# Performance work log

Measured on AMD Instinct MI355X. Metric: run time of the kernel, lower is better.

The kernel has to match this reference:

```python
import jax, jax.numpy as jnp
import numpy as np

B, S, E, H = 2, 2048, 1024, 16
D = E // H  # head dim = 64

def setup_inputs() -> dict:
    key = jax.random.key(0)
    ks = jax.random.split(key, 7)
    mk = lambda k, shape, scale=1.0: (jax.random.normal(k, shape, dtype=jnp.float32) * scale)
    return {
        "query": mk(ks[0], (B, S, E)),
        "key": mk(ks[1], (B, S, E)),
        "value": mk(ks[2], (B, S, E)),
        "Wq": mk(ks[3], (E, E), 1.0 / np.sqrt(E)),
        "Wk": mk(ks[4], (E, E), 1.0 / np.sqrt(E)),
        "Wv": mk(ks[5], (E, E), 1.0 / np.sqrt(E)),
        "Wo": mk(ks[6], (E, E), 1.0 / np.sqrt(E)),
    }

def reference(query, key, value, Wq, Wk, Wv, Wo):
    # nn.Linear(bias=False): y = x @ W.T
    def split_heads(x):
        return x.reshape(B, -1, H, D).transpose(0, 2, 1, 3)  # [B,H,S,D]
    q = split_heads(query @ Wq.T)
    k = split_heads(key @ Wk.T)
    v = split_heads(value @ Wv.T)
    scores = jnp.einsum("bhqd,bhkd->bhqk", q, k) / jnp.sqrt(jnp.float32(D))
    attn = jax.nn.softmax(scores, axis=-1)  # dropout p=0 -> identity
    out = jnp.einsum("bhqk,bhkd->bhqd", attn, v)
    out = out.transpose(0, 2, 1, 3).reshape(B, -1, E)
    out = out @ Wo.T
    return out
```

## Files before the change

kernel.cpp:

```cpp
#include <hip/hip_runtime.h>
#include <stdint.h>

#define S_LEN 2048
#define HDIM  64
#define EMB   1024
#define NTOK  4096

typedef short bf16x8 __attribute__((ext_vector_type(8)));
typedef float f32x4  __attribute__((ext_vector_type(4)));

__device__ __forceinline__ unsigned short f32_bf16(float f) {
  union { float f; uint32_t u; } v; v.f = f;
  return (unsigned short)((v.u + 0x7fffu + ((v.u >> 16) & 1u)) >> 16);
}

__device__ __forceinline__ uint32_t fbits(float f) {
  union { float f; uint32_t u; } v; v.f = f; return v.u;
}

__device__ __forceinline__ uint32_t pack_bf16_trunc(float lo, float hi) {
  return __builtin_amdgcn_perm(fbits(hi), fbits(lo), 0x07060302u);
}

__device__ __forceinline__ void async_ld16(const unsigned short* g, unsigned short* l) {
  __builtin_amdgcn_global_load_lds(
      (__attribute__((address_space(1))) unsigned int*)(uintptr_t)g,
      (__attribute__((address_space(3))) unsigned int*)l, 16, 0, 0);
}

#define CL2 0.18033688f

__global__ void cast_all(const float* __restrict__ q, const float* __restrict__ k,
                         const float* __restrict__ v, const float* __restrict__ Wq,
                         const float* __restrict__ Wk, const float* __restrict__ Wv,
                         const float* __restrict__ Wo,
                         unsigned short* __restrict__ qb, unsigned short* __restrict__ kb,
                         unsigned short* __restrict__ vb, unsigned short* __restrict__ wqb,
                         unsigned short* __restrict__ wkb, unsigned short* __restrict__ wvb,
                         unsigned short* __restrict__ wob) {
  const int b = blockIdx.x;
  const float* src; unsigned short* dst; int base;
  float scl = 1.0f;
  if (b < 12288) {
    const int which = b >> 12; base = b & 4095;
    src = which == 0 ? q : which == 1 ? k : v;
    dst = which == 0 ? qb : which == 1 ? kb : vb;
  } else {
    const int bb = b - 12288, which = bb >> 10; base = bb & 1023;
    src = which == 0 ? Wq : which == 1 ? Wk : which == 2 ? Wv : Wo;
    dst = which == 0 ? wqb : which == 1 ? wkb : which == 2 ? wvb : wob;
    if (which == 0) scl = CL2;
  }
  const int i = base * 256 + threadIdx.x;
  float4 f = ((const float4*)src)[i];
  ushort4 o;
  o.x = f32_bf16(f.x * scl); o.y = f32_bf16(f.y * scl);
  o.z = f32_bf16(f.z * scl); o.w = f32_bf16(f.w * scl);
  ((ushort4*)dst)[i] = o;
}

__device__ __forceinline__ void gemm_core(const unsigned short* __restrict__ A,
                                          const unsigned short* __restrict__ Bw,
                                          unsigned short* As, unsigned short* Bs,
                                          int tileM, int tileN, f32x4 (&acc)[4][4]) {
  const int tid  = threadIdx.x;
  const int lane = tid & 63;
  const int wave = tid >> 6;
  const int wm = (wave >> 1) * 64;
  const int wn = (wave & 1) * 64;
  const int ccol = lane & 15;
  const int cgrp = lane >> 4;
  const int rchunk = lane >> 2;
  const int coff   = (lane & 3) * 8;

  for (int k0 = 0; k0 < EMB; k0 += 32) {
#pragma unroll
    for (int i = 0; i < 2; ++i) {
      const int c = wave * 2 + i;
      const int row = c * 16 + rchunk;
      async_ld16(A  + (size_t)(tileM + row) * EMB + k0 + coff, As + c * 512);
      async_ld16(Bw + (size_t)(tileN + row) * EMB + k0 + coff, Bs + c * 512);
    }
    __syncthreads();
    bf16x8 af[4], bfm[4];
#pragma unroll
    for (int i = 0; i < 4; ++i) {
      af[i]  = *(const bf16x8*)(As + (wm + i * 16 + ccol) * 32 + cgrp * 8);
      bfm[i] = *(const bf16x8*)(Bs + (wn + i * 16 + ccol) * 32 + cgrp * 8);
    }
#pragma unroll
    for (int i = 0; i < 4; ++i)
#pragma unroll
      for (int j = 0; j < 4; ++j)
        acc[i][j] = __builtin_amdgcn_mfma_f32_16x16x32_bf16(af[i], bfm[j], acc[i][j], 0, 0, 0);
    __syncthreads();
  }
}

__global__ __launch_bounds__(256)
void gemm_qkv(const unsigned short* __restrict__ qb, const unsigned short* __restrict__ kb,
              const unsigned short* __restrict__ vb, const unsigned short* __restrict__ wqb,
              const unsigned short* __restrict__ wkb, const unsigned short* __restrict__ wvb,
              unsigned short* __restrict__ Qh, unsigned short* __restrict__ Kh,
              unsigned short* __restrict__ Vt) {
  extern __shared__ __align__(16) char smem_raw[];
  unsigned short* As = (unsigned short*)smem_raw;
  unsigned short* Bs = As + 128 * 32;
  unsigned short* Ct = Bs + 128 * 32;

  const int z = blockIdx.z;
  const unsigned short* A  = z == 0 ? qb  : z == 1 ? kb  : vb;
  const unsigned short* Bw = z == 0 ? wqb : z == 1 ? wkb : wvb;
  const int tileM = blockIdx.y * 128;
  const int tileN = blockIdx.x * 128;

  f32x4 acc[4][4];
#pragma unroll
  for (int i = 0; i < 4; ++i)
#pragma unroll
    for (int j = 0; j < 4; ++j) acc[i][j] = 0.f;

  gemm_core(A, Bw, As, Bs, tileM, tileN, acc);

  const int tid = threadIdx.x, lane = tid & 63, wave = tid >> 6;
  const int wm = (wave >> 1) * 64, wn = (wave & 1) * 64;
  const int ccol = lane & 15, cgrp = lane >> 4;

  if (z < 2) {
    unsigned short* Oh = (z == 0) ? Qh : Kh;
#pragma unroll
    for (int i = 0; i < 4; ++i) {
      const int rbase = tileM + wm + i * 16 + cgrp * 4;
#pragma unroll
      for (int j = 0; j < 4; ++j) {
        const int gcol = tileN + wn + j * 16 + ccol;
        const int h = gcol >> 6, dd = gcol & 63;
#pragma unroll
        for (int r = 0; r < 4; ++r) {
          const int grow = rbase + r;
          const int b = grow >> 11, s = grow & 2047;
          Oh[((size_t)((b * 16 + h) * 2048 + s)) * 64 + dd] = f32_bf16(acc[i][j][r]);
        }
      }
    }
  } else {
#pragma unroll
    for (int i = 0; i < 4; ++i)
#pragma unroll
      for (int j = 0; j < 4; ++j)
#pragma unroll
        for (int r = 0; r < 4; ++r)
          Ct[(wm + i * 16 + cgrp * 4 + r) * 130 + (wn + j * 16 + ccol)] = f32_bf16(acc[i][j][r]);
    __syncthreads();
#pragma unroll 4
    for (int it = 0; it < 64; ++it) {
      const int flat = it * 256 + tid;
      const int c  = flat >> 7;
      const int rl = flat & 127;
      const int gcol = tileN + c, grow = tileM + rl;
      const int h = gcol >> 6, dd = gcol & 63;
      const int b = grow >> 11, s = grow & 2047;
      Vt[((size_t)((b * 16 + h) * 64 + dd)) * 2048 + s] = Ct[rl * 130 + c];
    }
  }
}

__global__ __launch_bounds__(256)
void gemm_out(const unsigned short* __restrict__ A, const unsigned short* __restrict__ Bw,
              float* __restrict__ Out) {
  __shared__ __align__(16) unsigned short As[128 * 32];
  __shared__ __align__(16) unsigned short Bs[64 * 32];

  const int tid  = threadIdx.x;
  const int lane = tid & 63;
  const int wave = tid >> 6;
  const int wm = (wave >> 1) * 64;
  const int wn = (wave & 1) * 32;
  const int ccol = lane & 15;
  const int cgrp = lane >> 4;
  const int rchunk = lane >> 2;
  const int coff   = (lane & 3) * 8;
  const int tileM = blockIdx.y * 128;
  const int tileN = blockIdx.x * 64;

  f32x4 acc[4][2];
#pragma unroll
  for (int i = 0; i < 4; ++i)
#pragma unroll
    for (int j = 0; j < 2; ++j) acc[i][j] = 0.f;

  for (int k0 = 0; k0 < EMB; k0 += 32) {
#pragma unroll
    for (int i = 0; i < 2; ++i) {
      const int c = wave * 2 + i;
      const int row = c * 16 + rchunk;
      async_ld16(A + (size_t)(tileM + row) * EMB + k0 + coff, As + c * 512);
    }
    {
      const int row = wave * 16 + rchunk;
      async_ld16(Bw + (size_t)(tileN + row) * EMB + k0 + coff, Bs + wave * 512);
    }
    __syncthreads();
    bf16x8 af[4], bfm[2];
#pragma unroll
    for (int i = 0; i < 4; ++i)
      af[i] = *(const bf16x8*)(As + (wm + i * 16 + ccol) * 32 + cgrp * 8);
#pragma unroll
    for (int j = 0; j < 2; ++j)
      bfm[j] = *(const bf16x8*)(Bs + (wn + j * 16 + ccol) * 32 + cgrp * 8);
#pragma unroll
    for (int i = 0; i < 4; ++i)
#pragma unroll
      for (int j = 0; j < 2; ++j)
        acc[i][j] = __builtin_amdgcn_mfma_f32_16x16x32_bf16(af[i], bfm[j], acc[i][j], 0, 0, 0);
    __syncthreads();
  }

#pragma unroll
  for (int i = 0; i < 4; ++i) {
    const int rbase = tileM + wm + i * 16 + cgrp * 4;
#pragma unroll
    for (int j = 0; j < 2; ++j) {
      const int gcol = tileN + wn + j * 16 + ccol;
#pragma unroll
      for (int r = 0; r < 4; ++r)
        Out[(size_t)(rbase + r) * 1024 + gcol] = acc[i][j][r];
    }
  }
}

__global__ __launch_bounds__(256, 4)
void attn_kernel(const unsigned short* __restrict__ Qh,
                 const unsigned short* __restrict__ Kh,
                 const unsigned short* __restrict__ Vt,
                 unsigned short* __restrict__ Ctx) {
  __shared__ __align__(16) unsigned short Ks[2 * 64 * 64];
  __shared__ __align__(16) unsigned short Vs[2 * 64 * 64];
  __shared__ __align__(16) unsigned short Ps[4 * 16 * 64];

  const int tid  = threadIdx.x;
  const int lane = tid & 63;
  const int wave = tid >> 6;
  const int bh = blockIdx.y;
  const int q0 = blockIdx.x * 64;
  const unsigned short* Qg = Qh + ((size_t)bh * S_LEN + q0) * HDIM;
  const unsigned short* Kg = Kh + (size_t)bh * S_LEN * HDIM;
  const unsigned short* Vg = Vt + (size_t)bh * HDIM * S_LEN;

  const int ccol = lane & 15;
  const int cgrp = lane >> 4;
  const int mrow = wave * 16;
  const int sw7  = ccol & 7;

#pragma unroll
  for (int i = 0; i < 2; ++i) {
    const int cid = i * 256 + tid;
    const int row = cid >> 3, j = cid & 7, g = j ^ (row & 7);
    *(int4*)&Ps[row * 64 + j * 8] = *(const int4*)&Qg[(size_t)row * 64 + g * 8];
  }
  __syncthreads();
  bf16x8 aq[2];
#pragma unroll
  for (int kk = 0; kk < 2; ++kk) {
    const int pp = (kk * 4 + cgrp) ^ sw7;
    aq[kk] = *(const bf16x8*)&Ps[(mrow + ccol) * 64 + pp * 8];
  }
  unsigned short* Pw = Ps + wave * 1024;

  const int r0 = tid >> 3, j0 = tid & 7;
  const int r1 = r0 + 32;
  const int sA = j0 ^ (r0 & 7);
  const int sB = j0 ^ (r1 & 7);

  int4 kr0 = *(const int4*)&Kg[(size_t)r0 * 64 + sA * 8];
  int4 kr1 = *(const int4*)&Kg[(size_t)r1 * 64 + sB * 8];
  int4 vr0 = *(const int4*)&Vg[(size_t)r0 * 2048 + sA * 8];
  int4 vr1 = *(const int4*)&Vg[(size_t)r1 * 2048 + sB * 8];

  f32x4 l4 = 0.f;
  f32x4 o_acc[4];
#pragma unroll
  for (int dt = 0; dt < 4; ++dt) o_acc[dt] = 0.f;

  for (int i = 0; i < 32; ++i) {
    unsigned short* Kb = Ks + (i & 1) * 4096;
    unsigned short* Vb = Vs + (i & 1) * 4096;
    *(int4*)&Kb[r0 * 64 + j0 * 8] = kr0;
    *(int4*)&Kb[r1 * 64 + j0 * 8] = kr1;
    *(int4*)&Vb[r0 * 64 + j0 * 8] = vr0;
    *(int4*)&Vb[r1 * 64 + j0 * 8] = vr1;
    __syncthreads();
    if (i < 31) {
      const int nb = (i + 1) * 64;
      kr0 = *(const int4*)&Kg[(size_t)(nb + r0) * 64 + sA * 8];
      kr1 = *(const int4*)&Kg[(size_t)(nb + r1) * 64 + sB * 8];
      vr0 = *(const int4*)&Vg[(size_t)r0 * 2048 + nb + sA * 8];
      vr1 = *(const int4*)&Vg[(size_t)r1 * 2048 + nb + sB * 8];
    }

    f32x4 sc[4];
#pragma unroll
    for (int nt = 0; nt < 4; ++nt) {
      f32x4 s = 0.f;
#pragma unroll
      for (int kk = 0; kk < 2; ++kk) {
        const int krow = nt * 16 + ccol;
        const int c8 = (kk * 4 + cgrp) ^ (krow & 7);
        bf16x8 ak = *(const bf16x8*)&Kb[krow * 64 + c8 * 8];
        s = __builtin_amdgcn_mfma_f32_16x16x32_bf16(ak, aq[kk], s, 0, 0, 0);
      }
      sc[nt] = s;
    }

#pragma unroll
    for (int nt = 0; nt < 4; ++nt) {
#pragma unroll
      for (int r = 0; r < 4; ++r)
        sc[nt][r] = __builtin_amdgcn_exp2f(sc[nt][r]);
      l4 += sc[nt];
    }

#pragma unroll
    for (int nt = 0; nt < 4; ++nt) {
      const uint32_t u0 = pack_bf16_trunc(sc[nt][0], sc[nt][1]);
      const uint32_t u1 = pack_bf16_trunc(sc[nt][2], sc[nt][3]);
      const int pp = (nt * 2 + (cgrp >> 1)) ^ sw7;
      *(int2*)&Pw[ccol * 64 + pp * 8 + (cgrp & 1) * 4] = make_int2((int)u0, (int)u1);
    }
    asm volatile("s_waitcnt lgkmcnt(0)" ::: "memory");
    bf16x8 ap[2];
#pragma unroll
    for (int kk = 0; kk < 2; ++kk) {
      const int pp = (kk * 4 + cgrp) ^ sw7;
      ap[kk] = *(const bf16x8*)&Pw[ccol * 64 + pp * 8];
    }

#pragma unroll
    for (int dt = 0; dt < 4; ++dt) {
      f32x4 o = o_acc[dt];
#pragma unroll
      for (int kk = 0; kk < 2; ++kk) {
        const int vrow = dt * 16 + ccol;
        const int c8 = (kk * 4 + cgrp) ^ (vrow & 7);
        bf16x8 av = *(const bf16x8*)&Vb[vrow * 64 + c8 * 8];
        o = __builtin_amdgcn_mfma_f32_16x16x32_bf16(av, ap[kk], o, 0, 0, 0);
      }
      o_acc[dt] = o;
    }
  }

  float l_i = l4[0] + l4[1] + l4[2] + l4[3];
  l_i += __shfl_xor(l_i, 16);
  l_i += __shfl_xor(l_i, 32);
  const int b = bh >> 4, h = bh & 15;
  const float inv_l = __builtin_amdgcn_rcpf(l_i) * 1.00195f;
  const int srow = q0 + mrow + ccol;
#pragma unroll
  for (int dt = 0; dt < 4; ++dt) {
    float o0 = o_acc[dt][0] * inv_l, o1 = o_acc[dt][1] * inv_l;
    float o2 = o_acc[dt][2] * inv_l, o3 = o_acc[dt][3] * inv_l;
    uint32_t u0 = (uint32_t)f32_bf16(o0) | ((uint32_t)f32_bf16(o1) << 16);
    uint32_t u1 = (uint32_t)f32_bf16(o2) | ((uint32_t)f32_bf16(o3) << 16);
    const int col = h * 64 + dt * 16 + cgrp * 4;
    *(int2*)&Ctx[((size_t)(b * 2048 + srow)) * 1024 + col] = make_int2((int)u0, (int)u1);
  }
}

extern "C" void kernel_launch(void* const* d_in, const int* in_sizes, int n_in,
                              void* d_out, int out_size, void* d_ws, size_t ws_size,
                              hipStream_t stream) {
  const float* q  = (const float*)d_in[0];
  const float* k  = (const float*)d_in[1];
  const float* v  = (const float*)d_in[2];
  const float* Wq = (const float*)d_in[3];
  const float* Wk = (const float*)d_in[4];
  const float* Wv = (const float*)d_in[5];
  const float* Wo = (const float*)d_in[6];

  const size_t tok = (size_t)NTOK * EMB;
  const size_t wsz = (size_t)EMB * EMB;
  unsigned short* p = (unsigned short*)d_ws;
  unsigned short* qb  = p; p += tok;
  unsigned short* kb  = p; p += tok;
  unsigned short* vb  = p; p += tok;
  unsigned short* wqb = p; p += wsz;
  unsigned short* wkb = p; p += wsz;
  unsigned short* wvb = p; p += wsz;
  unsigned short* wob = p; p += wsz;
  unsigned short* Qh  = p; p += tok;
  unsigned short* Kh  = p; p += tok;
  unsigned short* Vt  = p; p += tok;
  unsigned short* Ctx = p; p += tok;

  cast_all<<<dim3(16384), dim3(256), 0, stream>>>(q, k, v, Wq, Wk, Wv, Wo,
                                                  qb, kb, vb, wqb, wkb, wvb, wob);

  const size_t smem_qkv = 128 * 32 * 2 * 2 + 128 * 130 * 2;
  gemm_qkv<<<dim3(8, 32, 3), dim3(256), smem_qkv, stream>>>(qb, kb, vb, wqb, wkb, wvb,
                                                            Qh, Kh, Vt);

  attn_kernel<<<dim3(32, 32), dim3(256), 0, stream>>>(Qh, Kh, Vt, Ctx);

  gemm_out<<<dim3(16, 32), dim3(256), 0, stream>>>(Ctx, wob, (float*)d_out);
}
```

Before: 241.9 us.

## Swap GEMM operand roles in QKV projection to vectorize head-layout stores

For Q and K the projection is now computed transposed (weights as the A operand, tokens as B), so each lane's four accumulator rows map to consecutive head-dim elements and can be written as one 8-byte store. For V the original orientation already puts consecutive tokens in a lane's accumulator, so Vt is written directly with packed 8-byte stores and the LDS transpose staging buffer plus its barrier are removed. This lowers shared memory use and replaces scattered 2-byte global writes with wider ones. Stores are still strided across lanes, so coalescing is only partial.

Result: faster. 222.8 us (-7.9%).

```diff
diff --git a/kernel.cpp b/kernel.cpp
--- a/kernel.cpp
+++ b/kernel.cpp
@@ -20,6 +20,10 @@
 
 __device__ __forceinline__ uint32_t pack_bf16_trunc(float lo, float hi) {
   return __builtin_amdgcn_perm(fbits(hi), fbits(lo), 0x07060302u);
+}
+
+__device__ __forceinline__ uint32_t pack_bf16_rne(float lo, float hi) {
+  return (uint32_t)f32_bf16(lo) | ((uint32_t)f32_bf16(hi) << 16);
 }
 
 __device__ __forceinline__ void async_ld16(const unsigned short* g, unsigned short* l) {
@@ -103,16 +107,19 @@
               const unsigned short* __restrict__ wkb, const unsigned short* __restrict__ wvb,
               unsigned short* __restrict__ Qh, unsigned short* __restrict__ Kh,
               unsigned short* __restrict__ Vt) {
-  extern __shared__ __align__(16) char smem_raw[];
-  unsigned short* As = (unsigned short*)smem_raw;
-  unsigned short* Bs = As + 128 * 32;
-  unsigned short* Ct = Bs + 128 * 32;
-
-  const int z = blockIdx.z;
-  const unsigned short* A  = z == 0 ? qb  : z == 1 ? kb  : vb;
-  const unsigned short* Bw = z == 0 ? wqb : z == 1 ? wkb : wvb;
-  const int tileM = blockIdx.y * 128;
-  const int tileN = blockIdx.x * 128;
+  __shared__ __align__(16) unsigned short As[128 * 32];
+  __shared__ __align__(16) unsigned short Bs[128 * 32];
+
+  const int z  = blockIdx.z;
+  const int bx = blockIdx.x;
+  const int by = blockIdx.y;
+  const unsigned short* Xp = z == 0 ? qb  : z == 1 ? kb  : vb;
+  const unsigned short* Wp = z == 0 ? wqb : z == 1 ? wkb : wvb;
+
+  const unsigned short *A, *B;
+  int tileM, tileN;
+  if (z < 2) { A = Wp; tileM = bx * 128; B = Xp; tileN = by * 128; }
+  else       { A = Xp; tileM = by * 128; B = Wp; tileN = bx * 128; }
 
   f32x4 acc[4][4];
 #pragma unroll
@@ -120,7 +127,7 @@
 #pragma unroll
     for (int j = 0; j < 4; ++j) acc[i][j] = 0.f;
 
-  gemm_core(A, Bw, As, Bs, tileM, tileN, acc);
+  gemm_core(A, B, As, Bs, tileM, tileN, acc);
 
   const int tid = threadIdx.x, lane = tid & 63, wave = tid >> 6;
   const int wm = (wave >> 1) * 64, wn = (wave & 1) * 64;
@@ -130,37 +137,32 @@
     unsigned short* Oh = (z == 0) ? Qh : Kh;
 #pragma unroll
     for (int i = 0; i < 4; ++i) {
-      const int rbase = tileM + wm + i * 16 + cgrp * 4;
+      const int gd = tileM + wm + i * 16 + cgrp * 4;
+      const int h = gd >> 6, dd = gd & 63;
 #pragma unroll
       for (int j = 0; j < 4; ++j) {
-        const int gcol = tileN + wn + j * 16 + ccol;
-        const int h = gcol >> 6, dd = gcol & 63;
-#pragma unroll
-        for (int r = 0; r < 4; ++r) {
-          const int grow = rbase + r;
-          const int b = grow >> 11, s = grow & 2047;
-          Oh[((size_t)((b * 16 + h) * 2048 + s)) * 64 + dd] = f32_bf16(acc[i][j][r]);
-        }
+        const int gt = tileN + wn + j * 16 + ccol;
+        const int b = gt >> 11, s = gt & 2047;
+        const uint32_t u0 = pack_bf16_rne(acc[i][j][0], acc[i][j][1]);
+        const uint32_t u1 = pack_bf16_rne(acc[i][j][2], acc[i][j][3]);
+        *(int2*)&Oh[((size_t)((b * 16 + h) * 2048 + s)) * 64 + dd] =
+            make_int2((int)u0, (int)u1);
       }
     }
   } else {
 #pragma unroll
-    for (int i = 0; i < 4; ++i)
-#pragma unroll
-      for (int j = 0; j < 4; ++j)
-#pragma unroll
-        for (int r = 0; r < 4; ++r)
-          Ct[(wm + i * 16 + cgrp * 4 + r) * 130 + (wn + j * 16 + ccol)] = f32_bf16(acc[i][j][r]);
-    __syncthreads();
-#pragma unroll 4
-    for (int it = 0; it < 64; ++it) {
-      const int flat = it * 256 + tid;
-      const int c  = flat >> 7;
-      const int rl = flat & 127;
-      const int gcol = tileN + c, grow = tileM + rl;
-      const int h = gcol >> 6, dd = gcol & 63;
-      const int b = grow >> 11, s = grow & 2047;
-      Vt[((size_t)((b * 16 + h) * 64 + dd)) * 2048 + s] = Ct[rl * 130 + c];
+    for (int i = 0; i < 4; ++i) {
+      const int gt = tileM + wm + i * 16 + cgrp * 4;
+      const int b = gt >> 11, s = gt & 2047;
+#pragma unroll
+      for (int j = 0; j < 4; ++j) {
+        const int gd = tileN + wn + j * 16 + ccol;
+        const int h = gd >> 6, dd = gd & 63;
+        const uint32_t u0 = pack_bf16_rne(acc[i][j][0], acc[i][j][1]);
+        const uint32_t u1 = pack_bf16_rne(acc[i][j][2], acc[i][j][3]);
+        *(int2*)&Vt[((size_t)((b * 16 + h) * 64 + dd)) * 2048 + s] =
+            make_int2((int)u0, (int)u1);
+      }
     }
   }
 }
@@ -359,8 +361,8 @@
   for (int dt = 0; dt < 4; ++dt) {
     float o0 = o_acc[dt][0] * inv_l, o1 = o_acc[dt][1] * inv_l;
     float o2 = o_acc[dt][2] * inv_l, o3 = o_acc[dt][3] * inv_l;
-    uint32_t u0 = (uint32_t)f32_bf16(o0) | ((uint32_t)f32_bf16(o1) << 16);
-    uint32_t u1 = (uint32_t)f32_bf16(o2) | ((uint32_t)f32_bf16(o3) << 16);
+    uint32_t u0 = pack_bf16_rne(o0, o1);
+    uint32_t u1 = pack_bf16_rne(o2, o3);
     const int col = h * 64 + dt * 16 + cgrp * 4;
     *(int2*)&Ctx[((size_t)(b * 2048 + srow)) * 1024 + col] = make_int2((int)u0, (int)u1);
   }
@@ -395,9 +397,8 @@
   cast_all<<<dim3(16384), dim3(256), 0, stream>>>(q, k, v, Wq, Wk, Wv, Wo,
                                                   qb, kb, vb, wqb, wkb, wvb, wob);
 
-  const size_t smem_qkv = 128 * 32 * 2 * 2 + 128 * 130 * 2;
-  gemm_qkv<<<dim3(8, 32, 3), dim3(256), smem_qkv, stream>>>(qb, kb, vb, wqb, wkb, wvb,
-                                                            Qh, Kh, Vt);
+  gemm_qkv<<<dim3(8, 32, 3), dim3(256), 0, stream>>>(qb, kb, vb, wqb, wkb, wvb,
+                                                     Qh, Kh, Vt);
 
   attn_kernel<<<dim3(32, 32), dim3(256), 0, stream>>>(Qh, Kh, Vt, Ctx);
 
```
